# Optimization experiments

Hardware: AMD Instinct MI355X
Metric: run time of the kernel (lower is better)

Reference implementation:

```python
import jax, jax.numpy as jnp
import numpy as np

N = 128        # num nodes == num activities (required by the flatten->linear coupling)
F_IN = 256     # num_node_features
H = 512        # graph_conv_layer_sizes
E = 524288     # number of edges
D0, D1 = 512, 256  # dense_layer_sizes


def _edge_conv(x, src, dst, W1, b1, W2, b2):
    # gather endpoints per edge: x_i = target, x_j = source (PyG source_to_target flow)
    x_i = x[dst]                      # [E, C]
    x_j = x[src]                      # [E, C]
    t = jnp.concatenate([x_i, x_j - x_i], axis=1)          # [E, 2C]
    m = jnp.dot(jax.nn.relu(jnp.dot(t, W1) + b1), W2) + b2  # [E, H]
    agg = jax.ops.segment_max(m, dst, num_segments=N)       # scatter-max into targets
    # PyG fills empty segments with 0; segment_max yields -inf for empty segments
    return jnp.where(jnp.isfinite(agg), agg, 0.0)


def setup_inputs() -> dict:
    key = jax.random.key(0)
    ks = jax.random.split(key, 16)

    def w(k, shape, fan_in):
        return (jax.random.normal(k, shape, jnp.float32) / np.float32(np.sqrt(fan_in)))

    return {
        "x": jax.random.normal(ks[0], (N, F_IN), jnp.float32),
        "edge_index": jax.random.randint(ks[1], (2, E), 0, N, dtype=jnp.int32),
        # EdgeConv 1: Linear(2*F_IN -> H), ReLU, Linear(H -> H)
        "c1_W1": w(ks[2], (2 * F_IN, H), 2 * F_IN), "c1_b1": jnp.zeros((H,), jnp.float32),
        "c1_W2": w(ks[3], (H, H), H),               "c1_b2": jnp.zeros((H,), jnp.float32),
        # EdgeConv 2: Linear(2*H -> H), ReLU, Linear(H -> H)
        "c2_W1": w(ks[4], (2 * H, H), 2 * H),       "c2_b1": jnp.zeros((H,), jnp.float32),
        "c2_W2": w(ks[5], (H, H), H),               "c2_b2": jnp.zeros((H,), jnp.float32),
        # dense head on flattened [N*H] vector
        "lin_W": w(ks[6], (N * H, D0), N * H),      "lin_b": jnp.zeros((D0,), jnp.float32),
        "lin1_W": w(ks[7], (D0, D1), D0),           "lin1_b": jnp.zeros((D1,), jnp.float32),
        "out_W": w(ks[8], (D1, N), D1),             "out_b": jnp.zeros((N,), jnp.float32),
    }


def reference(x, edge_index, c1_W1, c1_b1, c1_W2, c1_b2,
              c2_W1, c2_b1, c2_W2, c2_b2,
              lin_W, lin_b, lin1_W, lin1_b, out_W, out_b):
    src, dst = edge_index[0], edge_index[1]
    h = jax.nn.relu(_edge_conv(x, src, dst, c1_W1, c1_b1, c1_W2, c1_b2))
    h = jax.nn.relu(_edge_conv(h, src, dst, c2_W1, c2_b1, c2_W2, c2_b2))
    v = h.reshape(-1)                       # torch.flatten; dropout is identity in eval
    v = jax.nn.relu(jnp.dot(v, lin_W) + lin_b)
    v = jax.nn.relu(jnp.dot(v, lin1_W) + lin1_b)
    v = jax.nn.relu(jnp.dot(v, out_W) + out_b)
    return jax.nn.softmax(v, axis=0)
```

## Files before the change

### kernel.cpp

```cpp
#include <hip/hip_runtime.h>
#include <cfloat>
#include <cmath>
#include <cstdint>

#define N_NODES 128
#define F_IN    256
#define HDIM    512
#define NEDGE   524288

typedef _Float16 half8 __attribute__((ext_vector_type(8)));
typedef _Float16 half4 __attribute__((ext_vector_type(4)));
typedef float f32x4 __attribute__((ext_vector_type(4)));

__global__ __launch_bounds__(256) void prep_kernel(
    const int* __restrict__ ei, unsigned int* __restrict__ mask,
    const float* __restrict__ W2a, const float* __restrict__ W2b,
    _Float16* __restrict__ Ta, _Float16* __restrict__ Tb) {
  __shared__ __align__(16) char smem[64 * 72 * 2];
  const int t = threadIdx.x;
  if (blockIdx.x < 256) {
    unsigned int* lm = (unsigned int*)smem;
    for (int i = t; i < N_NODES * 4; i += 256) lm[i] = 0u;
    __syncthreads();
    const int base = blockIdx.x * 2048;
#pragma unroll
    for (int r = 0; r < 8; ++r) {
      const int e = base + r * 256 + t;
      const int s = ei[e];
      const int d = ei[NEDGE + e];
      atomicOr(&lm[d * 4 + (s >> 5)], 1u << (s & 31));
    }
    __syncthreads();
    for (int i = t; i < N_NODES * 4; i += 256) {
      const unsigned int v = lm[i];
      if (v) atomicOr(&mask[i], v);
    }
  } else {
    const int b = blockIdx.x - 256;
    const int layer = b >> 6;
    const int rem = b & 63;
    const int kb = (rem & 7) * 64;
    const int nb = (rem >> 3) * 64;
    const float* W = layer ? W2b : W2a;
    _Float16* T = layer ? Tb : Ta;
    _Float16(*tile)[72] = (_Float16(*)[72])smem;
#pragma unroll
    for (int i = 0; i < 4; ++i) {
      const int slot = t + i * 256;
      const int kk = slot >> 4;
      const int nq = (slot & 15) * 4;
      const float4 w4 = *reinterpret_cast<const float4*>(
          &W[(size_t)(kb + kk) * HDIM + nb + nq]);
      tile[nq + 0][kk] = (_Float16)w4.x;
      tile[nq + 1][kk] = (_Float16)w4.y;
      tile[nq + 2][kk] = (_Float16)w4.z;
      tile[nq + 3][kk] = (_Float16)w4.w;
    }
    __syncthreads();
#pragma unroll
    for (int i = 0; i < 2; ++i) {
      const int slot = t + i * 256;
      const int n = slot >> 3;
      const int ko = (slot & 7) * 8;
      *reinterpret_cast<half8*>(&T[(size_t)(nb + n) * HDIM + kb + ko]) =
          *reinterpret_cast<const half8*>(&tile[n][ko]);
    }
  }
}

template <int KK>
__global__ __launch_bounds__(256) void uv_gemm4_kernel(
    const float* __restrict__ A, const float* __restrict__ W,
    const float* __restrict__ bias, float* __restrict__ U,
    float* __restrict__ V) {
  constexpr int S = 4;
  constexpr int KS = KK / S;
  constexpr int BK = 32;
  __shared__ float As[128][BK + 1];
  __shared__ float Wd[BK][20];
  __shared__ float Wb[BK][20];
  const int t = threadIdx.x;
  const int tx = t & 3;
  const int ty = t >> 2;
  const int h0 = blockIdx.x * 16;
  const int ks0 = blockIdx.y * KS;

  float accU[2][4], accV[2][4];
#pragma unroll
  for (int i = 0; i < 2; ++i)
#pragma unroll
    for (int j = 0; j < 4; ++j) { accU[i][j] = 0.f; accV[i][j] = 0.f; }

  for (int ch = 0; ch < KS / BK; ++ch) {
    const int k0 = ks0 + ch * BK;
    __syncthreads();
#pragma unroll
    for (int i = 0; i < 4; ++i) {
      const int slot = t + i * 256;
      const int dd = slot >> 3, kw = (slot & 7) * 4;
      const float4 a4 =
          *reinterpret_cast<const float4*>(&A[dd * KK + k0 + kw]);
      As[dd][kw + 0] = a4.x;
      As[dd][kw + 1] = a4.y;
      As[dd][kw + 2] = a4.z;
      As[dd][kw + 3] = a4.w;
    }
    if (t < 128) {
      const int k = t >> 2, hq = (t & 3) * 4;
      const float4 wt = *reinterpret_cast<const float4*>(
          &W[(size_t)(k0 + k) * HDIM + h0 + hq]);
      const float4 wb = *reinterpret_cast<const float4*>(
          &W[(size_t)(KK + k0 + k) * HDIM + h0 + hq]);
      *reinterpret_cast<float4*>(&Wb[k][hq]) = wb;
      float4 wd;
      wd.x = wt.x - wb.x; wd.y = wt.y - wb.y;
      wd.z = wt.z - wb.z; wd.w = wt.w - wb.w;
      *reinterpret_cast<float4*>(&Wd[k][hq]) = wd;
    }
    __syncthreads();
#pragma unroll
    for (int k = 0; k < BK; ++k) {
      float a[2];
#pragma unroll
      for (int i = 0; i < 2; ++i) a[i] = As[ty * 2 + i][k];
      const float4 wd4 = *reinterpret_cast<const float4*>(&Wd[k][tx * 4]);
      const float4 wb4 = *reinterpret_cast<const float4*>(&Wb[k][tx * 4]);
      const float wdv[4] = {wd4.x, wd4.y, wd4.z, wd4.w};
      const float wbv[4] = {wb4.x, wb4.y, wb4.z, wb4.w};
#pragma unroll
      for (int i = 0; i < 2; ++i)
#pragma unroll
        for (int j = 0; j < 4; ++j) {
          accU[i][j] = fmaf(a[i], wdv[j], accU[i][j]);
          accV[i][j] = fmaf(a[i], wbv[j], accV[i][j]);
        }
    }
  }
  const int cbase = h0 + tx * 4;
  float bb[4] = {0.f, 0.f, 0.f, 0.f};
  if (blockIdx.y == 0) {
#pragma unroll
    for (int j = 0; j < 4; ++j) bb[j] = bias[cbase + j];
  }
#pragma unroll
  for (int i = 0; i < 2; ++i) {
    const int row = ty * 2 + i;
#pragma unroll
    for (int j = 0; j < 4; ++j) {
      atomicAdd(&U[row * HDIM + cbase + j], accU[i][j] + bb[j]);
      atomicAdd(&V[row * HDIM + cbase + j], accV[i][j]);
    }
  }
}

#define PBK 64
__global__ __launch_bounds__(256) void pair_mfma_kernel(
    const float* __restrict__ U, const float* __restrict__ V,
    const _Float16* __restrict__ W2t, const float* __restrict__ b2,
    const unsigned int* __restrict__ mask, float* __restrict__ out) {
  __shared__ _Float16 As[128][PBK + 8];
  __shared__ _Float16 Bs[128][PBK + 8];
  __shared__ float Ur[HDIM];
  __shared__ float red[4][128];
  const int t = threadIdx.x;
  const int d = blockIdx.y;
  const int c0 = blockIdx.x * 128;
  const int lane = t & 63;
  const int wid = t >> 6;
  const int l15 = lane & 15;
  const int quad = lane >> 4;

  for (int i = t; i < HDIM; i += 256) Ur[i] = U[d * HDIM + i];
  const unsigned int mwv[4] = {mask[d * 4 + 0], mask[d * 4 + 1],
                               mask[d * 4 + 2], mask[d * 4 + 3]};

  f32x4 acc[8][2];
#pragma unroll
  for (int mt = 0; mt < 8; ++mt)
#pragma unroll
    for (int nt = 0; nt < 2; ++nt) acc[mt][nt] = (f32x4)(0.f);

  for (int ch = 0; ch < HDIM / PBK; ++ch) {
    const int k0 = ch * PBK;
    __syncthreads();
#pragma unroll
    for (int i = 0; i < 8; ++i) {
      const int slot = t + i * 256;
      const int s = slot >> 4;
      const int kq = (slot & 15) * 4;
      const float4 v4 =
          *reinterpret_cast<const float4*>(&V[s * HDIM + k0 + kq]);
      const float4 u4 = *reinterpret_cast<const float4*>(&Ur[k0 + kq]);
      half4 h;
      h.x = (_Float16)fmaxf(u4.x + v4.x, 0.f);
      h.y = (_Float16)fmaxf(u4.y + v4.y, 0.f);
      h.z = (_Float16)fmaxf(u4.z + v4.z, 0.f);
      h.w = (_Float16)fmaxf(u4.w + v4.w, 0.f);
      *reinterpret_cast<half4*>(&As[s][kq]) = h;
    }
#pragma unroll
    for (int i = 0; i < 4; ++i) {
      const int slot = t + i * 256;
      const int n = slot >> 3;
      const int ko = (slot & 7) * 8;
      *reinterpret_cast<half8*>(&Bs[n][ko]) = *reinterpret_cast<const half8*>(
          &W2t[(size_t)(c0 + n) * HDIM + k0 + ko]);
    }
    __syncthreads();
#pragma unroll
    for (int ks = 0; ks < PBK / 32; ++ks) {
      half8 bf[2];
#pragma unroll
      for (int nt = 0; nt < 2; ++nt)
        bf[nt] = *reinterpret_cast<const half8*>(
            &Bs[wid * 32 + nt * 16 + l15][ks * 32 + quad * 8]);
#pragma unroll
      for (int mt = 0; mt < 8; ++mt) {
        const half8 af = *reinterpret_cast<const half8*>(
            &As[mt * 16 + l15][ks * 32 + quad * 8]);
#pragma unroll
        for (int nt = 0; nt < 2; ++nt)
          acc[mt][nt] = __builtin_amdgcn_mfma_f32_16x16x32_f16(
              af, bf[nt], acc[mt][nt], 0, 0, 0);
      }
    }
  }
  __syncthreads();
#pragma unroll
  for (int nt = 0; nt < 2; ++nt) {
    float pm = -FLT_MAX;
#pragma unroll
    for (int mt = 0; mt < 8; ++mt) {
      const int sbase = mt * 16 + quad * 4;
      const unsigned int w = mwv[sbase >> 5] >> (sbase & 31);
#pragma unroll
      for (int r = 0; r < 4; ++r)
        if ((w >> r) & 1u) pm = fmaxf(pm, acc[mt][nt][r]);
    }
    red[quad][wid * 32 + nt * 16 + l15] = pm;
  }
  __syncthreads();
  if (t < 128) {
    const float m = fmaxf(fmaxf(red[0][t], red[1][t]),
                          fmaxf(red[2][t], red[3][t]));
    out[d * HDIM + c0 + t] = fmaxf(m + b2[c0 + t], 0.f);
  }
}

__global__ __launch_bounds__(256) void head_gemv4_kernel(
    const float* __restrict__ v, const float* __restrict__ W,
    float* __restrict__ z0r) {
  __shared__ float vs[128];
  __shared__ float red[4][512];
  const int t = threadIdx.x;
  const int b = blockIdx.x;
  const int row0 = b * 128;
  if (t < 128) vs[t] = v[row0 + t];
  __syncthreads();
  const int w = t >> 6;
  const int l = t & 63;
  const float* Wp = W + (size_t)row0 * 512 + l * 8;
  float4 accA = make_float4(0.f, 0.f, 0.f, 0.f);
  float4 accB = make_float4(0.f, 0.f, 0.f, 0.f);
#pragma unroll
  for (int bb = 0; bb < 4; ++bb) {
    const int r0 = w * 32 + bb * 8;
    float4 wa[8], wb[8];
#pragma unroll
    for (int i = 0; i < 8; ++i) {
      const float* p = Wp + (size_t)(r0 + i) * 512;
      wa[i] = *reinterpret_cast<const float4*>(p);
      wb[i] = *reinterpret_cast<const float4*>(p + 4);
    }
#pragma unroll
    for (int i = 0; i < 8; ++i) {
      const float x = vs[r0 + i];
      accA.x = fmaf(x, wa[i].x, accA.x);
      accA.y = fmaf(x, wa[i].y, accA.y);
      accA.z = fmaf(x, wa[i].z, accA.z);
      accA.w = fmaf(x, wa[i].w, accA.w);
      accB.x = fmaf(x, wb[i].x, accB.x);
      accB.y = fmaf(x, wb[i].y, accB.y);
      accB.z = fmaf(x, wb[i].z, accB.z);
      accB.w = fmaf(x, wb[i].w, accB.w);
    }
  }
  *reinterpret_cast<float4*>(&red[w][l * 8]) = accA;
  *reinterpret_cast<float4*>(&red[w][l * 8 + 4]) = accB;
  __syncthreads();
  float* zr = z0r + (size_t)(b & 7) * 512;
  const float s0 = red[0][t] + red[1][t] + red[2][t] + red[3][t];
  const int c2 = t + 256;
  const float s1 = red[0][c2] + red[1][c2] + red[2][c2] + red[3][c2];
  atomicAdd(&zr[t], s0);
  atomicAdd(&zr[c2], s1);
}

__global__ __launch_bounds__(512) void head_tail_kernel(
    const float* __restrict__ z0r, const float* __restrict__ lin_b,
    const float* __restrict__ lin1W, const float* __restrict__ lin1b,
    const float* __restrict__ outW, const float* __restrict__ outb,
    float* __restrict__ out) {
  __shared__ float zr[512];
  __shared__ float r1[2][256];
  __shared__ float z1s[256];
  __shared__ float r2[4][128];
  __shared__ float z2s[128];
  __shared__ float rr[128];
  const int t = threadIdx.x;
  {
    float s = 0.f;
#pragma unroll
    for (int r = 0; r < 8; ++r) s += z0r[r * 512 + t];
    zr[t] = fmaxf(s + lin_b[t], 0.f);
  }
  __syncthreads();
  {
    const int c = t & 255;
    const int kh = t >> 8;
    float acc = 0.f;
#pragma unroll
    for (int b2 = 0; b2 < 16; ++b2) {
      const int k0 = kh * 256 + b2 * 16;
      float wv[16];
#pragma unroll
      for (int i = 0; i < 16; ++i) wv[i] = lin1W[(size_t)(k0 + i) * 256 + c];
#pragma unroll
      for (int i = 0; i < 16; ++i) acc = fmaf(zr[k0 + i], wv[i], acc);
    }
    r1[kh][c] = acc;
  }
  __syncthreads();
  if (t < 256) z1s[t] = fmaxf(r1[0][t] + r1[1][t] + lin1b[t], 0.f);
  __syncthreads();
  {
    const int c = t & 127;
    const int kq = t >> 7;
    float acc = 0.f;
#pragma unroll
    for (int b2 = 0; b2 < 4; ++b2) {
      const int k0 = kq * 64 + b2 * 16;
      float wv[16];
#pragma unroll
      for (int i = 0; i < 16; ++i) wv[i] = outW[(size_t)(k0 + i) * 128 + c];
#pragma unroll
      for (int i = 0; i < 16; ++i) acc = fmaf(z1s[k0 + i], wv[i], acc);
    }
    r2[kq][c] = acc;
  }
  __syncthreads();
  if (t < 128) {
    const float z =
        fmaxf(r2[0][t] + r2[1][t] + r2[2][t] + r2[3][t] + outb[t], 0.f);
    z2s[t] = z;
    rr[t] = z;
  }
  __syncthreads();
  for (int off = 64; off > 0; off >>= 1) {
    if (t < off) rr[t] = fmaxf(rr[t], rr[t + off]);
    __syncthreads();
  }
  const float mx = rr[0];
  __syncthreads();
  if (t < 128) {
    const float e = expf(z2s[t] - mx);
    z2s[t] = e;
    rr[t] = e;
  }
  __syncthreads();
  for (int off = 64; off > 0; off >>= 1) {
    if (t < off) rr[t] += rr[t + off];
    __syncthreads();
  }
  if (t < 128) out[t] = z2s[t] / rr[0];
}

extern "C" void kernel_launch(void* const* d_in, const int* in_sizes, int n_in,
                              void* d_out, int out_size, void* d_ws,
                              size_t ws_size, hipStream_t stream) {
  const float* x      = (const float*)d_in[0];
  const int*   ei     = (const int*)d_in[1];
  const float* c1_W1  = (const float*)d_in[2];
  const float* c1_b1  = (const float*)d_in[3];
  const float* c1_W2  = (const float*)d_in[4];
  const float* c1_b2  = (const float*)d_in[5];
  const float* c2_W1  = (const float*)d_in[6];
  const float* c2_b1  = (const float*)d_in[7];
  const float* c2_W2  = (const float*)d_in[8];
  const float* c2_b2  = (const float*)d_in[9];
  const float* lin_W  = (const float*)d_in[10];
  const float* lin_b  = (const float*)d_in[11];
  const float* lin1_W = (const float*)d_in[12];
  const float* lin1_b = (const float*)d_in[13];
  const float* out_W  = (const float*)d_in[14];
  const float* out_b  = (const float*)d_in[15];
  float* out = (float*)d_out;

  char* wsb = (char*)d_ws;
  unsigned int* mask = (unsigned int*)wsb;
  float* z0r = (float*)(wsb + 2048);
  float* U1 = z0r + 4096;
  float* V1 = U1 + 65536;
  float* U2 = V1 + 65536;
  float* V2 = U2 + 65536;
  const size_t zero_bytes = 2048 + 4096 * 4 + 4 * 65536 * 4;
  float* h1 = V2 + 65536;
  float* h2 = h1 + 65536;
  _Float16* W2t1 = (_Float16*)(h2 + 65536);
  _Float16* W2t2 = W2t1 + 262144;

  hipMemsetAsync(wsb, 0, zero_bytes, stream);
  prep_kernel<<<384, 256, 0, stream>>>(ei, mask, c1_W2, c2_W2, W2t1, W2t2);
  uv_gemm4_kernel<256><<<dim3(32, 4), 256, 0, stream>>>(x, c1_W1, c1_b1, U1, V1);
  pair_mfma_kernel<<<dim3(4, 128), 256, 0, stream>>>(U1, V1, W2t1, c1_b2, mask, h1);
  uv_gemm4_kernel<512><<<dim3(32, 4), 256, 0, stream>>>(h1, c2_W1, c2_b1, U2, V2);
  pair_mfma_kernel<<<dim3(4, 128), 256, 0, stream>>>(U2, V2, W2t2, c2_b2, mask, h2);
  head_gemv4_kernel<<<512, 256, 0, stream>>>(h2, lin_W, z0r);
  head_tail_kernel<<<1, 512, 0, stream>>>(z0r, lin_b, lin1_W, lin1_b, out_W,
                                          out_b, out);
}
```

Measured before the change: 315.7 us.

## Fuse prep with first UV GEMM and head GEMV into second pair kernel

Result: no change. 317.9 us (+0.7%).

```diff
diff --git a/kernel.cpp b/kernel.cpp
--- a/kernel.cpp
+++ b/kernel.cpp
@@ -12,78 +12,20 @@
 typedef _Float16 half4 __attribute__((ext_vector_type(4)));
 typedef float f32x4 __attribute__((ext_vector_type(4)));
 
-__global__ __launch_bounds__(256) void prep_kernel(
-    const int* __restrict__ ei, unsigned int* __restrict__ mask,
-    const float* __restrict__ W2a, const float* __restrict__ W2b,
-    _Float16* __restrict__ Ta, _Float16* __restrict__ Tb) {
-  __shared__ __align__(16) char smem[64 * 72 * 2];
-  const int t = threadIdx.x;
-  if (blockIdx.x < 256) {
-    unsigned int* lm = (unsigned int*)smem;
-    for (int i = t; i < N_NODES * 4; i += 256) lm[i] = 0u;
-    __syncthreads();
-    const int base = blockIdx.x * 2048;
-#pragma unroll
-    for (int r = 0; r < 8; ++r) {
-      const int e = base + r * 256 + t;
-      const int s = ei[e];
-      const int d = ei[NEDGE + e];
-      atomicOr(&lm[d * 4 + (s >> 5)], 1u << (s & 31));
-    }
-    __syncthreads();
-    for (int i = t; i < N_NODES * 4; i += 256) {
-      const unsigned int v = lm[i];
-      if (v) atomicOr(&mask[i], v);
-    }
-  } else {
-    const int b = blockIdx.x - 256;
-    const int layer = b >> 6;
-    const int rem = b & 63;
-    const int kb = (rem & 7) * 64;
-    const int nb = (rem >> 3) * 64;
-    const float* W = layer ? W2b : W2a;
-    _Float16* T = layer ? Tb : Ta;
-    _Float16(*tile)[72] = (_Float16(*)[72])smem;
-#pragma unroll
-    for (int i = 0; i < 4; ++i) {
-      const int slot = t + i * 256;
-      const int kk = slot >> 4;
-      const int nq = (slot & 15) * 4;
-      const float4 w4 = *reinterpret_cast<const float4*>(
-          &W[(size_t)(kb + kk) * HDIM + nb + nq]);
-      tile[nq + 0][kk] = (_Float16)w4.x;
-      tile[nq + 1][kk] = (_Float16)w4.y;
-      tile[nq + 2][kk] = (_Float16)w4.z;
-      tile[nq + 3][kk] = (_Float16)w4.w;
-    }
-    __syncthreads();
-#pragma unroll
-    for (int i = 0; i < 2; ++i) {
-      const int slot = t + i * 256;
-      const int n = slot >> 3;
-      const int ko = (slot & 7) * 8;
-      *reinterpret_cast<half8*>(&T[(size_t)(nb + n) * HDIM + kb + ko]) =
-          *reinterpret_cast<const half8*>(&tile[n][ko]);
-    }
-  }
-}
-
-template <int KK>
-__global__ __launch_bounds__(256) void uv_gemm4_kernel(
+template <int KK, int S>
+__device__ __forceinline__ void uv_body(
     const float* __restrict__ A, const float* __restrict__ W,
     const float* __restrict__ bias, float* __restrict__ U,
-    float* __restrict__ V) {
-  constexpr int S = 4;
+    float* __restrict__ V, const int h0, const int ks0, const bool addb,
+    char* smem) {
   constexpr int KS = KK / S;
   constexpr int BK = 32;
-  __shared__ float As[128][BK + 1];
-  __shared__ float Wd[BK][20];
-  __shared__ float Wb[BK][20];
+  float(*As)[BK + 1] = (float(*)[BK + 1])smem;
+  float(*Wd)[20] = (float(*)[20])(smem + 128 * (BK + 1) * 4);
+  float(*Wb)[20] = (float(*)[20])(smem + 128 * (BK + 1) * 4 + BK * 20 * 4);
   const int t = threadIdx.x;
   const int tx = t & 3;
   const int ty = t >> 2;
-  const int h0 = blockIdx.x * 16;
-  const int ks0 = blockIdx.y * KS;
 
   float accU[2][4], accV[2][4];
 #pragma unroll
@@ -138,7 +80,7 @@
   }
   const int cbase = h0 + tx * 4;
   float bb[4] = {0.f, 0.f, 0.f, 0.f};
-  if (blockIdx.y == 0) {
+  if (addb) {
 #pragma unroll
     for (int j = 0; j < 4; ++j) bb[j] = bias[cbase + j];
   }
@@ -153,15 +95,92 @@
   }
 }
 
+__global__ __launch_bounds__(256) void prep_uv1_kernel(
+    const int* __restrict__ ei, unsigned int* __restrict__ mask,
+    const float* __restrict__ W2a, const float* __restrict__ W2b,
+    _Float16* __restrict__ Ta, _Float16* __restrict__ Tb,
+    const float* __restrict__ x, const float* __restrict__ W1,
+    const float* __restrict__ b1, float* __restrict__ U1,
+    float* __restrict__ V1) {
+  __shared__ __align__(16) char smem[22016];
+  const int bx = blockIdx.x;
+  const int t = threadIdx.x;
+  if (bx < 128) {
+    const int hx = bx & 31, ky = bx >> 5;
+    uv_body<F_IN, 4>(x, W1, b1, U1, V1, hx * 16, ky * (F_IN / 4),
+                     ky == 0, smem);
+  } else if (bx < 384) {
+    unsigned int* lm = (unsigned int*)smem;
+    for (int i = t; i < N_NODES * 4; i += 256) lm[i] = 0u;
+    __syncthreads();
+    const int base = (bx - 128) * 2048;
+#pragma unroll
+    for (int r = 0; r < 8; ++r) {
+      const int e = base + r * 256 + t;
+      const int s = ei[e];
+      const int d = ei[NEDGE + e];
+      atomicOr(&lm[d * 4 + (s >> 5)], 1u << (s & 31));
+    }
+    __syncthreads();
+    for (int i = t; i < N_NODES * 4; i += 256) {
+      const unsigned int v = lm[i];
+      if (v) atomicOr(&mask[i], v);
+    }
+  } else {
+    const int b = bx - 384;
+    const int layer = b >> 6;
+    const int rem = b & 63;
+    const int kb = (rem & 7) * 64;
+    const int nb = (rem >> 3) * 64;
+    const float* W = layer ? W2b : W2a;
+    _Float16* T = layer ? Tb : Ta;
+    _Float16(*tile)[72] = (_Float16(*)[72])smem;
+#pragma unroll
+    for (int i = 0; i < 4; ++i) {
+      const int slot = t + i * 256;
+      const int kk = slot >> 4;
+      const int nq = (slot & 15) * 4;
+      const float4 w4 = *reinterpret_cast<const float4*>(
+          &W[(size_t)(kb + kk) * HDIM + nb + nq]);
+      tile[nq + 0][kk] = (_Float16)w4.x;
+      tile[nq + 1][kk] = (_Float16)w4.y;
+      tile[nq + 2][kk] = (_Float16)w4.z;
+      tile[nq + 3][kk] = (_Float16)w4.w;
+    }
+    __syncthreads();
+#pragma unroll
+    for (int i = 0; i < 2; ++i) {
+      const int slot = t + i * 256;
+      const int n = slot >> 3;
+      const int ko = (slot & 7) * 8;
+      *reinterpret_cast<half8*>(&T[(size_t)(nb + n) * HDIM + kb + ko]) =
+          *reinterpret_cast<const half8*>(&tile[n][ko]);
+    }
+  }
+}
+
+template <int KK, int S>
+__global__ __launch_bounds__(256) void uv_gemm_kernel(
+    const float* __restrict__ A, const float* __restrict__ W,
+    const float* __restrict__ bias, float* __restrict__ U,
+    float* __restrict__ V) {
+  __shared__ __align__(16) char smem[22016];
+  uv_body<KK, S>(A, W, bias, U, V, blockIdx.x * 16, blockIdx.y * (KK / S),
+                 blockIdx.y == 0, smem);
+}
+
 #define PBK 64
+template <bool FH>
 __global__ __launch_bounds__(256) void pair_mfma_kernel(
     const float* __restrict__ U, const float* __restrict__ V,
     const _Float16* __restrict__ W2t, const float* __restrict__ b2,
-    const unsigned int* __restrict__ mask, float* __restrict__ out) {
-  __shared__ _Float16 As[128][PBK + 8];
+    const unsigned int* __restrict__ mask, float* __restrict__ out,
+    const float* __restrict__ linW, float* __restrict__ z0r) {
+  __shared__ __align__(16) _Float16 As[128][PBK + 8];
   __shared__ _Float16 Bs[128][PBK + 8];
   __shared__ float Ur[HDIM];
   __shared__ float red[4][128];
+  __shared__ float vs[128];
   const int t = threadIdx.x;
   const int d = blockIdx.y;
   const int c0 = blockIdx.x * 128;
@@ -243,57 +262,54 @@
   if (t < 128) {
     const float m = fmaxf(fmaxf(red[0][t], red[1][t]),
                           fmaxf(red[2][t], red[3][t]));
-    out[d * HDIM + c0 + t] = fmaxf(m + b2[c0 + t], 0.f);
-  }
-}
-
-__global__ __launch_bounds__(256) void head_gemv4_kernel(
-    const float* __restrict__ v, const float* __restrict__ W,
-    float* __restrict__ z0r) {
-  __shared__ float vs[128];
-  __shared__ float red[4][512];
-  const int t = threadIdx.x;
-  const int b = blockIdx.x;
-  const int row0 = b * 128;
-  if (t < 128) vs[t] = v[row0 + t];
-  __syncthreads();
-  const int w = t >> 6;
-  const int l = t & 63;
-  const float* Wp = W + (size_t)row0 * 512 + l * 8;
-  float4 accA = make_float4(0.f, 0.f, 0.f, 0.f);
-  float4 accB = make_float4(0.f, 0.f, 0.f, 0.f);
-#pragma unroll
-  for (int bb = 0; bb < 4; ++bb) {
-    const int r0 = w * 32 + bb * 8;
-    float4 wa[8], wb[8];
-#pragma unroll
-    for (int i = 0; i < 8; ++i) {
-      const float* p = Wp + (size_t)(r0 + i) * 512;
-      wa[i] = *reinterpret_cast<const float4*>(p);
-      wb[i] = *reinterpret_cast<const float4*>(p + 4);
-    }
-#pragma unroll
-    for (int i = 0; i < 8; ++i) {
-      const float x = vs[r0 + i];
-      accA.x = fmaf(x, wa[i].x, accA.x);
-      accA.y = fmaf(x, wa[i].y, accA.y);
-      accA.z = fmaf(x, wa[i].z, accA.z);
-      accA.w = fmaf(x, wa[i].w, accA.w);
-      accB.x = fmaf(x, wb[i].x, accB.x);
-      accB.y = fmaf(x, wb[i].y, accB.y);
-      accB.z = fmaf(x, wb[i].z, accB.z);
-      accB.w = fmaf(x, wb[i].w, accB.w);
-    }
-  }
-  *reinterpret_cast<float4*>(&red[w][l * 8]) = accA;
-  *reinterpret_cast<float4*>(&red[w][l * 8 + 4]) = accB;
-  __syncthreads();
-  float* zr = z0r + (size_t)(b & 7) * 512;
-  const float s0 = red[0][t] + red[1][t] + red[2][t] + red[3][t];
-  const int c2 = t + 256;
-  const float s1 = red[0][c2] + red[1][c2] + red[2][c2] + red[3][c2];
-  atomicAdd(&zr[t], s0);
-  atomicAdd(&zr[c2], s1);
+    const float val = fmaxf(m + b2[c0 + t], 0.f);
+    if (FH) vs[t] = val;
+    else out[d * HDIM + c0 + t] = val;
+  }
+  if (FH) {
+    __syncthreads();
+    float* red2 = (float*)As;
+    const int w = t >> 6;
+    const int l = t & 63;
+    const size_t row0 = (size_t)d * HDIM + c0;
+    const float* Wp = linW + row0 * 512 + l * 8;
+    float4 accA = make_float4(0.f, 0.f, 0.f, 0.f);
+    float4 accB = make_float4(0.f, 0.f, 0.f, 0.f);
+#pragma unroll
+    for (int bb = 0; bb < 4; ++bb) {
+      const int r0 = w * 32 + bb * 8;
+      float4 wa[8], wb[8];
+#pragma unroll
+      for (int i = 0; i < 8; ++i) {
+        const float* p = Wp + (size_t)(r0 + i) * 512;
+        wa[i] = *reinterpret_cast<const float4*>(p);
+        wb[i] = *reinterpret_cast<const float4*>(p + 4);
+      }
+#pragma unroll
+      for (int i = 0; i < 8; ++i) {
+        const float xv = vs[r0 + i];
+        accA.x = fmaf(xv, wa[i].x, accA.x);
+        accA.y = fmaf(xv, wa[i].y, accA.y);
+        accA.z = fmaf(xv, wa[i].z, accA.z);
+        accA.w = fmaf(xv, wa[i].w, accA.w);
+        accB.x = fmaf(xv, wb[i].x, accB.x);
+        accB.y = fmaf(xv, wb[i].y, accB.y);
+        accB.z = fmaf(xv, wb[i].z, accB.z);
+        accB.w = fmaf(xv, wb[i].w, accB.w);
+      }
+    }
+    *reinterpret_cast<float4*>(&red2[w * 512 + l * 8]) = accA;
+    *reinterpret_cast<float4*>(&red2[w * 512 + l * 8 + 4]) = accB;
+    __syncthreads();
+    float* zr = z0r + (size_t)(((d << 2) | blockIdx.x) & 7) * 512;
+    const float s0 =
+        red2[t] + red2[512 + t] + red2[1024 + t] + red2[1536 + t];
+    const int cc = t + 256;
+    const float s1 =
+        red2[cc] + red2[512 + cc] + red2[1024 + cc] + red2[1536 + cc];
+    atomicAdd(&zr[t], s0);
+    atomicAdd(&zr[cc], s1);
+  }
 }
 
 __global__ __launch_bounds__(512) void head_tail_kernel(
@@ -405,17 +421,18 @@
   float* V2 = U2 + 65536;
   const size_t zero_bytes = 2048 + 4096 * 4 + 4 * 65536 * 4;
   float* h1 = V2 + 65536;
-  float* h2 = h1 + 65536;
-  _Float16* W2t1 = (_Float16*)(h2 + 65536);
+  _Float16* W2t1 = (_Float16*)(h1 + 65536);
   _Float16* W2t2 = W2t1 + 262144;
 
   hipMemsetAsync(wsb, 0, zero_bytes, stream);
-  prep_kernel<<<384, 256, 0, stream>>>(ei, mask, c1_W2, c2_W2, W2t1, W2t2);
-  uv_gemm4_kernel<256><<<dim3(32, 4), 256, 0, stream>>>(x, c1_W1, c1_b1, U1, V1);
-  pair_mfma_kernel<<<dim3(4, 128), 256, 0, stream>>>(U1, V1, W2t1, c1_b2, mask, h1);
-  uv_gemm4_kernel<512><<<dim3(32, 4), 256, 0, stream>>>(h1, c2_W1, c2_b1, U2, V2);
-  pair_mfma_kernel<<<dim3(4, 128), 256, 0, stream>>>(U2, V2, W2t2, c2_b2, mask, h2);
-  head_gemv4_kernel<<<512, 256, 0, stream>>>(h2, lin_W, z0r);
+  prep_uv1_kernel<<<512, 256, 0, stream>>>(ei, mask, c1_W2, c2_W2, W2t1, W2t2,
+                                           x, c1_W1, c1_b1, U1, V1);
+  pair_mfma_kernel<false><<<dim3(4, 128), 256, 0, stream>>>(
+      U1, V1, W2t1, c1_b2, mask, h1, nullptr, nullptr);
+  uv_gemm_kernel<512, 8><<<dim3(32, 8), 256, 0, stream>>>(h1, c2_W1, c2_b1,
+                                                          U2, V2);
+  pair_mfma_kernel<true><<<dim3(4, 128), 256, 0, stream>>>(
+      U2, V2, W2t2, c2_b2, mask, nullptr, lin_W, z0r);
   head_tail_kernel<<<1, 512, 0, stream>>>(z0r, lin_b, lin1_W, lin1_b, out_W,
                                           out_b, out);
 }
```
